# Optimization experiments

Hardware: AMD Instinct MI355X
Metric: run time of the kernel (lower is better)

## Reference

```python
import jax, jax.numpy as jnp
import numpy as np

B = 256          # graphs per batch
N = 128          # nodes per graph (equal-size graphs; batch is block-contiguous)
P = N * (N - 1) // 2  # pairs per graph = 8128
E = B * 1024     # total edges
D = 128          # node feature dim
L = 32           # latent dim

# precomputed local upper-triangular pair indices (constants)
_PI, _PJ = np.triu_indices(N, k=1)
_PI = jnp.asarray(_PI); _PJ = jnp.asarray(_PJ)


def setup_inputs() -> dict:
    key = jax.random.key(0)
    ks = jax.random.split(key, 8)
    x = jax.random.normal(ks[0], (B * N, D), dtype=jnp.float32)
    # within-graph edges with local i < j
    li = jax.random.randint(ks[1], (E,), 0, N - 1)
    r = jax.random.randint(ks[2], (E,), 0, 1 << 30)
    lj = li + 1 + r % (N - 1 - li)
    g = jax.random.randint(ks[3], (E,), 0, B)
    off = g * N
    edge_index = jnp.stack([off + li, off + lj]).astype(jnp.int64)
    batch = jnp.repeat(jnp.arange(B), N).astype(jnp.int64)
    eps = jax.random.normal(ks[4], (B * N, L), dtype=jnp.float32)
    W1 = jax.random.normal(ks[5], (D, D), dtype=jnp.float32) * 0.05
    b1 = jnp.zeros((D,), dtype=jnp.float32)
    Wmu = jax.random.normal(ks[6], (D, L), dtype=jnp.float32) * 0.05
    bmu = jnp.zeros((L,), dtype=jnp.float32)
    Wls = jax.random.normal(ks[7], (D, L), dtype=jnp.float32) * 0.05
    bls = jnp.zeros((L,), dtype=jnp.float32)
    return {"x": x, "edge_index": edge_index, "batch": batch, "eps": eps,
            "W1": W1, "b1": b1, "Wmu": Wmu, "bmu": bmu, "Wls": Wls, "bls": bls}


def reference(x, edge_index, batch, eps, W1, b1, Wmu, bmu, Wls, bls):
    src, dst = edge_index[0], edge_index[1]
    # --- encoder: one symmetric message-passing layer -> Gaussian q per node ---
    agg = jnp.zeros_like(x).at[dst].add(x[src]).at[src].add(x[dst])
    h = jax.nn.relu((x + agg) @ W1 + b1)
    mu = h @ Wmu + bmu                       # [BN, L]
    log_std = h @ Wls + bls
    std = jnp.exp(log_std)
    z = mu + std * eps                       # rsample
    # --- KL(q || N(0,I)) per node, summed per graph (kls[b]) ---
    kl_node = 0.5 * jnp.sum(std * std + mu * mu - 1.0 - 2.0 * log_std, axis=-1)
    kls = jax.ops.segment_sum(kl_node, batch, num_segments=B)  # [B]
    # --- link targets: scatter edges into triangular pair slots ---
    li, lj, be = src % N, dst % N, src // N
    pidx = li * (2 * N - li - 1) // 2 + (lj - li - 1)
    targets = jnp.zeros((B, P), dtype=z.dtype).at[be, pidx].set(1.0)
    # --- inner-product Bernoulli decoder over all pairs of every graph ---
    zb = z.reshape(B, N, L)
    logits = jnp.einsum('bpl,bpl->bp', zb[:, _PI], zb[:, _PJ])   # [B, P]
    log_probs = jnp.sum(targets * logits - jax.nn.softplus(logits), axis=-1)  # [B]
    elbo = jnp.mean(log_probs - kls)
    return -elbo
```

## Files before the change

kernel.cpp:

```cpp
#include <hip/hip_runtime.h>
#include <math.h>

#define B_ 256
#define N_ 128
#define D_ 128
#define L_ 32
#define E_ 262144
#define PW_ 254
#define DCAP 96

#define NDEG_OFF 0
#define BM_OFF   32768
#define KLS_OFF  97792
#define LP_OFF   98048
#define ADJ_OFF  98304
#define XA_OFF   884736
#define Z_OFF    5079040
#define ZERO_WORDS 98304

__global__ __launch_bounds__(256) void k_build(
    const int* __restrict__ ei, unsigned* __restrict__ ndeg,
    unsigned char* __restrict__ adj, unsigned* __restrict__ bm)
{
    int e = blockIdx.x * 256 + threadIdx.x;
    int src = ei[e], dst = ei[E_ + e];
    unsigned s1 = atomicAdd(&ndeg[src], 1u);
    if (s1 < DCAP) adj[(size_t)src * DCAP + s1] = (unsigned char)(dst & 127);
    unsigned s2 = atomicAdd(&ndeg[dst], 1u);
    if (s2 < DCAP) adj[(size_t)dst * DCAP + s2] = (unsigned char)(src & 127);
    int li = src & 127, lj = dst & 127, g = src >> 7;
    int p = li * (255 - li) / 2 + (lj - li - 1);
    atomicOr(&bm[g * PW_ + (p >> 5)], 1u << (p & 31));
}

__global__ __launch_bounds__(256) void k_aggregate(
    const float* __restrict__ x, const unsigned* __restrict__ ndeg,
    const unsigned char* __restrict__ adj, float* __restrict__ xa)
{
    int t = threadIdx.x;
    int grp = t >> 4;
    int l16 = t & 15;
    int gnode = blockIdx.x * 16 + grp;
    int gb = gnode & ~127;
    int fo = l16 * 8;

    const float* xr = x + (size_t)gnode * 128 + fo;
    float4 a0 = *(const float4*)xr;
    float4 a1 = *(const float4*)(xr + 4);

    int deg = (int)ndeg[gnode];
    if (deg > DCAP) deg = DCAP;
    const unsigned char* al = adj + (size_t)gnode * DCAP;

    int e = 0;
    for (; e + 4 <= deg; e += 4) {
        unsigned pk = *(const unsigned*)(al + e);
        int m0 = (int)(pk & 255u);
        int m1 = (int)((pk >> 8) & 255u);
        int m2 = (int)((pk >> 16) & 255u);
        int m3 = (int)(pk >> 24);
        const float* r0 = x + (size_t)(gb + m0) * 128 + fo;
        const float* r1 = x + (size_t)(gb + m1) * 128 + fo;
        const float* r2 = x + (size_t)(gb + m2) * 128 + fo;
        const float* r3 = x + (size_t)(gb + m3) * 128 + fo;
        float4 v00 = *(const float4*)r0, v01 = *(const float4*)(r0 + 4);
        float4 v10 = *(const float4*)r1, v11 = *(const float4*)(r1 + 4);
        float4 v20 = *(const float4*)r2, v21 = *(const float4*)(r2 + 4);
        float4 v30 = *(const float4*)r3, v31 = *(const float4*)(r3 + 4);
        a0.x += v00.x + v10.x + v20.x + v30.x;
        a0.y += v00.y + v10.y + v20.y + v30.y;
        a0.z += v00.z + v10.z + v20.z + v30.z;
        a0.w += v00.w + v10.w + v20.w + v30.w;
        a1.x += v01.x + v11.x + v21.x + v31.x;
        a1.y += v01.y + v11.y + v21.y + v31.y;
        a1.z += v01.z + v11.z + v21.z + v31.z;
        a1.w += v01.w + v11.w + v21.w + v31.w;
    }
    for (; e < deg; ++e) {
        int m = (int)al[e];
        const float* r = x + (size_t)(gb + m) * 128 + fo;
        float4 v0 = *(const float4*)r, v1 = *(const float4*)(r + 4);
        a0.x += v0.x; a0.y += v0.y; a0.z += v0.z; a0.w += v0.w;
        a1.x += v1.x; a1.y += v1.y; a1.z += v1.z; a1.w += v1.w;
    }
    float* o = xa + (size_t)gnode * 128 + fo;
    *(float4*)o = a0;
    *(float4*)(o + 4) = a1;
}

__global__ __launch_bounds__(256) void k_encoder(
    const float* __restrict__ xa, const float* __restrict__ W1,
    const float* __restrict__ b1, const float* __restrict__ Wmu,
    const float* __restrict__ bmu, const float* __restrict__ Wls,
    const float* __restrict__ bls, const float* __restrict__ eps,
    float* __restrict__ z, float* __restrict__ kls)
{
    __shared__ float XAs[64 * 132];
    __shared__ float Ws[8192];
    __shared__ float RED[256];
    int t = threadIdx.x;
    int row0 = blockIdx.x * 64;
    int g = blockIdx.x >> 1;
    int ty = t >> 4, tx = t & 15;

    #pragma unroll
    for (int i = 0; i < 8; ++i) {
        int c = t + i * 256;
        int n = c >> 5, d4 = (c & 31) << 2;
        *(float4*)(XAs + n * 132 + d4) = *(const float4*)(xa + (size_t)(row0 + n) * 128 + d4);
    }

    float acc[4][8];
    #pragma unroll
    for (int i = 0; i < 4; ++i)
        #pragma unroll
        for (int j = 0; j < 8; ++j) acc[i][j] = 0.f;

    for (int kh = 0; kh < 2; ++kh) {
        __syncthreads();
        #pragma unroll
        for (int i = 0; i < 8; ++i) {
            int c = t + i * 256;
            ((float4*)Ws)[c] = ((const float4*)(W1 + kh * 8192))[c];
        }
        __syncthreads();
        #pragma unroll 4
        for (int k = 0; k < 64; ++k) {
            int kk = kh * 64 + k;
            float a0 = XAs[(4 * ty + 0) * 132 + kk];
            float a1 = XAs[(4 * ty + 1) * 132 + kk];
            float a2 = XAs[(4 * ty + 2) * 132 + kk];
            float a3 = XAs[(4 * ty + 3) * 132 + kk];
            float4 w0 = *(const float4*)(Ws + k * 128 + 8 * tx);
            float4 w1 = *(const float4*)(Ws + k * 128 + 8 * tx + 4);
            float av[4] = {a0, a1, a2, a3};
            float wv[8] = {w0.x, w0.y, w0.z, w0.w, w1.x, w1.y, w1.z, w1.w};
            #pragma unroll
            for (int i = 0; i < 4; ++i)
                #pragma unroll
                for (int j = 0; j < 8; ++j) acc[i][j] += av[i] * wv[j];
        }
    }
    __syncthreads();

    {
        float4 bb0 = *(const float4*)(b1 + 8 * tx);
        float4 bb1 = *(const float4*)(b1 + 8 * tx + 4);
        float bb[8] = {bb0.x, bb0.y, bb0.z, bb0.w, bb1.x, bb1.y, bb1.z, bb1.w};
        #pragma unroll
        for (int i = 0; i < 4; ++i) {
            float4 h0, h1;
            h0.x = fmaxf(acc[i][0] + bb[0], 0.f);
            h0.y = fmaxf(acc[i][1] + bb[1], 0.f);
            h0.z = fmaxf(acc[i][2] + bb[2], 0.f);
            h0.w = fmaxf(acc[i][3] + bb[3], 0.f);
            h1.x = fmaxf(acc[i][4] + bb[4], 0.f);
            h1.y = fmaxf(acc[i][5] + bb[5], 0.f);
            h1.z = fmaxf(acc[i][6] + bb[6], 0.f);
            h1.w = fmaxf(acc[i][7] + bb[7], 0.f);
            *(float4*)(XAs + (4 * ty + i) * 132 + 8 * tx)     = h0;
            *(float4*)(XAs + (4 * ty + i) * 132 + 8 * tx + 4) = h1;
        }
    }
    #pragma unroll
    for (int i = 0; i < 8; ++i) {
        int c = t + i * 256;
        int row = c >> 4, col4 = (c & 15) << 2;
        float4 v = (col4 < 32) ? *(const float4*)(Wmu + row * 32 + col4)
                               : *(const float4*)(Wls + row * 32 + col4 - 32);
        *(float4*)(Ws + row * 64 + col4) = v;
    }
    __syncthreads();

    float a2c[4][4];
    #pragma unroll
    for (int i = 0; i < 4; ++i)
        #pragma unroll
        for (int j = 0; j < 4; ++j) a2c[i][j] = 0.f;
    #pragma unroll 4
    for (int k = 0; k < 128; ++k) {
        float h0 = XAs[(4 * ty + 0) * 132 + k];
        float h1 = XAs[(4 * ty + 1) * 132 + k];
        float h2 = XAs[(4 * ty + 2) * 132 + k];
        float h3 = XAs[(4 * ty + 3) * 132 + k];
        float4 wv = *(const float4*)(Ws + k * 64 + 4 * tx);
        float hv[4] = {h0, h1, h2, h3};
        float wa[4] = {wv.x, wv.y, wv.z, wv.w};
        #pragma unroll
        for (int i = 0; i < 4; ++i)
            #pragma unroll
            for (int j = 0; j < 4; ++j) a2c[i][j] += hv[i] * wa[j];
    }
    {
        float4 bv = (tx < 8) ? *(const float4*)(bmu + 4 * tx)
                             : *(const float4*)(bls + 4 * (tx - 8));
        float ba[4] = {bv.x, bv.y, bv.z, bv.w};
        #pragma unroll
        for (int i = 0; i < 4; ++i)
            #pragma unroll
            for (int j = 0; j < 4; ++j) a2c[i][j] += ba[j];
    }
    float oth[4][4];
    #pragma unroll
    for (int i = 0; i < 4; ++i)
        #pragma unroll
        for (int j = 0; j < 4; ++j) oth[i][j] = __shfl_xor(a2c[i][j], 8);

    float klsum = 0.f;
    {
        int i0 = (tx < 8) ? 0 : 2;
        int l0 = 4 * (tx & 7);
        #pragma unroll
        for (int ii = 0; ii < 2; ++ii) {
            int i = i0 + ii;
            int rowg = row0 + 4 * ty + i;
            float mu[4], lsv[4];
            #pragma unroll
            for (int j = 0; j < 4; ++j) {
                mu[j]  = (tx < 8) ? a2c[i][j] : oth[i][j];
                lsv[j] = (tx < 8) ? oth[i][j] : a2c[i][j];
            }
            float4 ev = *(const float4*)(eps + (size_t)rowg * 32 + l0);
            float ea[4] = {ev.x, ev.y, ev.z, ev.w};
            float4 zv;
            float zz[4];
            #pragma unroll
            for (int j = 0; j < 4; ++j) {
                float s = expf(lsv[j]);
                zz[j] = mu[j] + s * ea[j];
                klsum += s * s + mu[j] * mu[j] - 1.f - 2.f * lsv[j];
            }
            zv.x = zz[0]; zv.y = zz[1]; zv.z = zz[2]; zv.w = zz[3];
            *(float4*)(z + (size_t)rowg * 32 + l0) = zv;
        }
    }
    RED[t] = klsum;
    __syncthreads();
    for (int s = 128; s > 0; s >>= 1) {
        if (t < s) RED[t] += RED[t + s];
        __syncthreads();
    }
    if (t == 0) atomicAdd(&kls[g], 0.5f * RED[0]);
}

__global__ __launch_bounds__(256) void k_decoder(
    const float* __restrict__ z, const unsigned* __restrict__ bitmap,
    float* __restrict__ logp)
{
    __shared__ float zT[32 * 132];
    __shared__ unsigned bm[PW_];
    __shared__ float RED[256];
    int b = blockIdx.x >> 1, half = blockIdx.x & 1, t = threadIdx.x;

    #pragma unroll
    for (int i = 0; i < 16; ++i) {
        int c = t + i * 256;
        int n = c >> 5, l = c & 31;
        zT[l * 132 + n] = z[((size_t)b * N_ + n) * L_ + l];
    }
    if (t < PW_) bm[t] = bitmap[b * PW_ + t];
    __syncthreads();

    int i0 = half * 64 + ((t >> 5) << 3);
    int j0 = (t & 31) << 2;
    float g[8][4];
    #pragma unroll
    for (int a = 0; a < 8; ++a)
        #pragma unroll
        for (int c = 0; c < 4; ++c) g[a][c] = 0.f;

    #pragma unroll 4
    for (int l = 0; l < 32; ++l) {
        float4 a0 = *(const float4*)(zT + l * 132 + i0);
        float4 a1 = *(const float4*)(zT + l * 132 + i0 + 4);
        float4 b0 = *(const float4*)(zT + l * 132 + j0);
        float za[8] = {a0.x, a0.y, a0.z, a0.w, a1.x, a1.y, a1.z, a1.w};
        float zb[4] = {b0.x, b0.y, b0.z, b0.w};
        #pragma unroll
        for (int a = 0; a < 8; ++a)
            #pragma unroll
            for (int c = 0; c < 4; ++c) g[a][c] += za[a] * zb[c];
    }

    float sum = 0.f;
    #pragma unroll
    for (int a = 0; a < 8; ++a) {
        int i = i0 + a;
        #pragma unroll
        for (int c = 0; c < 4; ++c) {
            int j = j0 + c;
            if (j > i) {
                float lg = g[a][c];
                int p = i * (255 - i) / 2 + (j - i - 1);
                unsigned bit = (bm[p >> 5] >> (p & 31)) & 1u;
                float sp = log1pf(expf(-fabsf(lg))) + fmaxf(lg, 0.f);
                sum += bit ? (lg - sp) : (-sp);
            }
        }
    }
    RED[t] = sum;
    __syncthreads();
    for (int s = 128; s > 0; s >>= 1) {
        if (t < s) RED[t] += RED[t + s];
        __syncthreads();
    }
    if (t == 0) atomicAdd(&logp[b], RED[0]);
}

__global__ __launch_bounds__(256) void k_finalize(
    const float* __restrict__ kls, const float* __restrict__ logp,
    float* __restrict__ out)
{
    __shared__ float RED[256];
    int t = threadIdx.x;
    RED[t] = logp[t] - kls[t];
    __syncthreads();
    for (int s = 128; s > 0; s >>= 1) {
        if (t < s) RED[t] += RED[t + s];
        __syncthreads();
    }
    if (t == 0) out[0] = -RED[0] * (1.0f / 256.0f);
}

extern "C" void kernel_launch(void* const* d_in, const int* in_sizes, int n_in,
                              void* d_out, int out_size, void* d_ws, size_t ws_size,
                              hipStream_t stream) {
    const float* x   = (const float*)d_in[0];
    const int*   ei  = (const int*)d_in[1];
    const float* eps = (const float*)d_in[3];
    const float* W1  = (const float*)d_in[4];
    const float* b1  = (const float*)d_in[5];
    const float* Wmu = (const float*)d_in[6];
    const float* bmu = (const float*)d_in[7];
    const float* Wls = (const float*)d_in[8];
    const float* bls = (const float*)d_in[9];

    unsigned* wsw = (unsigned*)d_ws;
    unsigned*      ndeg = wsw + NDEG_OFF;
    unsigned*      bm   = wsw + BM_OFF;
    float*         kls  = (float*)(wsw + KLS_OFF);
    float*         logp = (float*)(wsw + LP_OFF);
    unsigned char* adj  = (unsigned char*)(wsw + ADJ_OFF);
    float*         xa   = (float*)(wsw + XA_OFF);
    float*         z    = (float*)(wsw + Z_OFF);

    hipMemsetAsync(d_ws, 0, ZERO_WORDS * sizeof(unsigned), stream);

    k_build    <<<E_ / 256, 256, 0, stream>>>(ei, ndeg, adj, bm);
    k_aggregate<<<(B_ * N_) / 16, 256, 0, stream>>>(x, ndeg, adj, xa);
    k_encoder  <<<512, 256, 0, stream>>>(xa, W1, b1, Wmu, bmu, Wls, bls,
                                         eps, z, kls);
    k_decoder  <<<2 * B_, 256, 0, stream>>>(z, bm, logp);
    k_finalize <<<1, 256, 0, stream>>>(kls, logp, (float*)d_out);
}
```

Before: 212.2 us.

## Fuse neighbor aggregation into encoder kernel and shrink weight smem tile

The separate aggregation kernel is removed. Each encoder block now gathers neighbor features for its 64 rows straight into shared memory, so the xa intermediate is never written to or read back from global memory and one launch disappears. The weight staging buffer is halved, with W1 loaded in four k-chunks and Wmu/Wls in two. This cuts shared memory per block to help occupancy, at the cost of more barriers. The gather now runs on only 512 blocks, which may expose gather latency.

```diff
diff --git a/kernel.cpp b/kernel.cpp
--- a/kernel.cpp
+++ b/kernel.cpp
@@ -14,8 +14,7 @@
 #define KLS_OFF  97792
 #define LP_OFF   98048
 #define ADJ_OFF  98304
-#define XA_OFF   884736
-#define Z_OFF    5079040
+#define Z_OFF    884736
 #define ZERO_WORDS 98304
 
 __global__ __launch_bounds__(256) void k_build(
@@ -33,82 +32,56 @@
     atomicOr(&bm[g * PW_ + (p >> 5)], 1u << (p & 31));
 }
 
-__global__ __launch_bounds__(256) void k_aggregate(
+__global__ __launch_bounds__(256) void k_encoder(
     const float* __restrict__ x, const unsigned* __restrict__ ndeg,
-    const unsigned char* __restrict__ adj, float* __restrict__ xa)
-{
-    int t = threadIdx.x;
-    int grp = t >> 4;
-    int l16 = t & 15;
-    int gnode = blockIdx.x * 16 + grp;
-    int gb = gnode & ~127;
-    int fo = l16 * 8;
-
-    const float* xr = x + (size_t)gnode * 128 + fo;
-    float4 a0 = *(const float4*)xr;
-    float4 a1 = *(const float4*)(xr + 4);
-
-    int deg = (int)ndeg[gnode];
-    if (deg > DCAP) deg = DCAP;
-    const unsigned char* al = adj + (size_t)gnode * DCAP;
-
-    int e = 0;
-    for (; e + 4 <= deg; e += 4) {
-        unsigned pk = *(const unsigned*)(al + e);
-        int m0 = (int)(pk & 255u);
-        int m1 = (int)((pk >> 8) & 255u);
-        int m2 = (int)((pk >> 16) & 255u);
-        int m3 = (int)(pk >> 24);
-        const float* r0 = x + (size_t)(gb + m0) * 128 + fo;
-        const float* r1 = x + (size_t)(gb + m1) * 128 + fo;
-        const float* r2 = x + (size_t)(gb + m2) * 128 + fo;
-        const float* r3 = x + (size_t)(gb + m3) * 128 + fo;
-        float4 v00 = *(const float4*)r0, v01 = *(const float4*)(r0 + 4);
-        float4 v10 = *(const float4*)r1, v11 = *(const float4*)(r1 + 4);
-        float4 v20 = *(const float4*)r2, v21 = *(const float4*)(r2 + 4);
-        float4 v30 = *(const float4*)r3, v31 = *(const float4*)(r3 + 4);
-        a0.x += v00.x + v10.x + v20.x + v30.x;
-        a0.y += v00.y + v10.y + v20.y + v30.y;
-        a0.z += v00.z + v10.z + v20.z + v30.z;
-        a0.w += v00.w + v10.w + v20.w + v30.w;
-        a1.x += v01.x + v11.x + v21.x + v31.x;
-        a1.y += v01.y + v11.y + v21.y + v31.y;
-        a1.z += v01.z + v11.z + v21.z + v31.z;
-        a1.w += v01.w + v11.w + v21.w + v31.w;
-    }
-    for (; e < deg; ++e) {
-        int m = (int)al[e];
-        const float* r = x + (size_t)(gb + m) * 128 + fo;
-        float4 v0 = *(const float4*)r, v1 = *(const float4*)(r + 4);
-        a0.x += v0.x; a0.y += v0.y; a0.z += v0.z; a0.w += v0.w;
-        a1.x += v1.x; a1.y += v1.y; a1.z += v1.z; a1.w += v1.w;
-    }
-    float* o = xa + (size_t)gnode * 128 + fo;
-    *(float4*)o = a0;
-    *(float4*)(o + 4) = a1;
-}
-
-__global__ __launch_bounds__(256) void k_encoder(
-    const float* __restrict__ xa, const float* __restrict__ W1,
-    const float* __restrict__ b1, const float* __restrict__ Wmu,
-    const float* __restrict__ bmu, const float* __restrict__ Wls,
-    const float* __restrict__ bls, const float* __restrict__ eps,
+    const unsigned char* __restrict__ adj,
+    const float* __restrict__ W1, const float* __restrict__ b1,
+    const float* __restrict__ Wmu, const float* __restrict__ bmu,
+    const float* __restrict__ Wls, const float* __restrict__ bls,
+    const float* __restrict__ eps,
     float* __restrict__ z, float* __restrict__ kls)
 {
     __shared__ float XAs[64 * 132];
-    __shared__ float Ws[8192];
+    __shared__ float Ws[4096];
     __shared__ float RED[256];
     int t = threadIdx.x;
     int row0 = blockIdx.x * 64;
     int g = blockIdx.x >> 1;
     int ty = t >> 4, tx = t & 15;
 
-    #pragma unroll
-    for (int i = 0; i < 8; ++i) {
-        int c = t + i * 256;
-        int n = c >> 5, d4 = (c & 31) << 2;
-        *(float4*)(XAs + n * 132 + d4) = *(const float4*)(xa + (size_t)(row0 + n) * 128 + d4);
-    }
+    {
+        int nidx = t >> 5;
+        int fo = (t & 31) << 2;
+        #pragma unroll 2
+        for (int p = 0; p < 8; ++p) {
+            int lrow = p * 8 + nidx;
+            int gnode = row0 + lrow;
+            const float* xr = x + (size_t)gnode * 128 + fo;
+            float4 acc = *(const float4*)xr;
+            int deg = (int)ndeg[gnode];
+            if (deg > DCAP) deg = DCAP;
+            const unsigned char* al = adj + (size_t)gnode * DCAP;
+            const float* gx = x + (size_t)(gnode & ~127) * 128 + fo;
+            int e = 0;
+            for (; e + 4 <= deg; e += 4) {
+                unsigned pk = *(const unsigned*)(al + e);
+                float4 v0 = *(const float4*)(gx + (pk & 255u) * 128);
+                float4 v1 = *(const float4*)(gx + ((pk >> 8) & 255u) * 128);
+                float4 v2 = *(const float4*)(gx + ((pk >> 16) & 255u) * 128);
+                float4 v3 = *(const float4*)(gx + (pk >> 24) * 128);
+                acc.x += v0.x + v1.x + v2.x + v3.x;
+                acc.y += v0.y + v1.y + v2.y + v3.y;
+                acc.z += v0.z + v1.z + v2.z + v3.z;
+                acc.w += v0.w + v1.w + v2.w + v3.w;
+            }
+            for (; e < deg; ++e) {
+                float4 v = *(const float4*)(gx + (unsigned)al[e] * 128);
+                acc.x += v.x; acc.y += v.y; acc.z += v.z; acc.w += v.w;
+            }
+            *(float4*)(XAs + lrow * 132 + fo) = acc;
+        }
+    }
+    __syncthreads();
 
     float acc[4][8];
     #pragma unroll
@@ -116,17 +89,17 @@
         #pragma unroll
         for (int j = 0; j < 8; ++j) acc[i][j] = 0.f;
 
-    for (int kh = 0; kh < 2; ++kh) {
-        __syncthreads();
-        #pragma unroll
-        for (int i = 0; i < 8; ++i) {
+    for (int kq = 0; kq < 4; ++kq) {
+        if (kq) __syncthreads();
+        #pragma unroll
+        for (int i = 0; i < 4; ++i) {
             int c = t + i * 256;
-            ((float4*)Ws)[c] = ((const float4*)(W1 + kh * 8192))[c];
+            ((float4*)Ws)[c] = ((const float4*)(W1 + kq * 4096))[c];
         }
         __syncthreads();
         #pragma unroll 4
-        for (int k = 0; k < 64; ++k) {
-            int kk = kh * 64 + k;
+        for (int k = 0; k < 32; ++k) {
+            int kk = kq * 32 + k;
             float a0 = XAs[(4 * ty + 0) * 132 + kk];
             float a1 = XAs[(4 * ty + 1) * 132 + kk];
             float a2 = XAs[(4 * ty + 2) * 132 + kk];
@@ -162,34 +135,39 @@
             *(float4*)(XAs + (4 * ty + i) * 132 + 8 * tx + 4) = h1;
         }
     }
-    #pragma unroll
-    for (int i = 0; i < 8; ++i) {
-        int c = t + i * 256;
-        int row = c >> 4, col4 = (c & 15) << 2;
-        float4 v = (col4 < 32) ? *(const float4*)(Wmu + row * 32 + col4)
-                               : *(const float4*)(Wls + row * 32 + col4 - 32);
-        *(float4*)(Ws + row * 64 + col4) = v;
-    }
-    __syncthreads();
 
     float a2c[4][4];
     #pragma unroll
     for (int i = 0; i < 4; ++i)
         #pragma unroll
         for (int j = 0; j < 4; ++j) a2c[i][j] = 0.f;
-    #pragma unroll 4
-    for (int k = 0; k < 128; ++k) {
-        float h0 = XAs[(4 * ty + 0) * 132 + k];
-        float h1 = XAs[(4 * ty + 1) * 132 + k];
-        float h2 = XAs[(4 * ty + 2) * 132 + k];
-        float h3 = XAs[(4 * ty + 3) * 132 + k];
-        float4 wv = *(const float4*)(Ws + k * 64 + 4 * tx);
-        float hv[4] = {h0, h1, h2, h3};
-        float wa[4] = {wv.x, wv.y, wv.z, wv.w};
-        #pragma unroll
-        for (int i = 0; i < 4; ++i)
-            #pragma unroll
-            for (int j = 0; j < 4; ++j) a2c[i][j] += hv[i] * wa[j];
+
+    for (int kh = 0; kh < 2; ++kh) {
+        __syncthreads();
+        #pragma unroll
+        for (int i = 0; i < 4; ++i) {
+            int c = t + i * 256;
+            int row = (c >> 4) + kh * 64, col4 = (c & 15) << 2;
+            float4 v = (col4 < 32) ? *(const float4*)(Wmu + row * 32 + col4)
+                                   : *(const float4*)(Wls + row * 32 + col4 - 32);
+            *(float4*)(Ws + (c >> 4) * 64 + col4) = v;
+        }
+        __syncthreads();
+        #pragma unroll 4
+        for (int k = 0; k < 64; ++k) {
+            int kk = kh * 64 + k;
+            float h0 = XAs[(4 * ty + 0) * 132 + kk];
+            float h1 = XAs[(4 * ty + 1) * 132 + kk];
+            float h2 = XAs[(4 * ty + 2) * 132 + kk];
+            float h3 = XAs[(4 * ty + 3) * 132 + kk];
+            float4 wv = *(const float4*)(Ws + k * 64 + 4 * tx);
+            float hv[4] = {h0, h1, h2, h3};
+            float wa[4] = {wv.x, wv.y, wv.z, wv.w};
+            #pragma unroll
+            for (int i = 0; i < 4; ++i)
+                #pragma unroll
+                for (int j = 0; j < 4; ++j) a2c[i][j] += hv[i] * wa[j];
+        }
     }
     {
         float4 bv = (tx < 8) ? *(const float4*)(bmu + 4 * tx)
@@ -341,15 +319,13 @@
     float*         kls  = (float*)(wsw + KLS_OFF);
     float*         logp = (float*)(wsw + LP_OFF);
     unsigned char* adj  = (unsigned char*)(wsw + ADJ_OFF);
-    float*         xa   = (float*)(wsw + XA_OFF);
     float*         z    = (float*)(wsw + Z_OFF);
 
     hipMemsetAsync(d_ws, 0, ZERO_WORDS * sizeof(unsigned), stream);
 
-    k_build    <<<E_ / 256, 256, 0, stream>>>(ei, ndeg, adj, bm);
-    k_aggregate<<<(B_ * N_) / 16, 256, 0, stream>>>(x, ndeg, adj, xa);
-    k_encoder  <<<512, 256, 0, stream>>>(xa, W1, b1, Wmu, bmu, Wls, bls,
-                                         eps, z, kls);
-    k_decoder  <<<2 * B_, 256, 0, stream>>>(z, bm, logp);
-    k_finalize <<<1, 256, 0, stream>>>(kls, logp, (float*)d_out);
-}
+    k_build   <<<E_ / 256, 256, 0, stream>>>(ei, ndeg, adj, bm);
+    k_encoder <<<512, 256, 0, stream>>>(x, ndeg, adj, W1, b1, Wmu, bmu,
+                                        Wls, bls, eps, z, kls);
+    k_decoder <<<2 * B_, 256, 0, stream>>>(z, bm, logp);
+    k_finalize<<<1, 256, 0, stream>>>(kls, logp, (float*)d_out);
+}
```

Result: no change. 209.4 us (-1.3%).
